# Performance work log

Hardware: AMD Instinct MI355X
Metric: run time of the kernel (lower is better)

Reference implementation:

```python
import jax, jax.numpy as jnp
import numpy as np

H, HD, RD = 16, 128, 64          # n_heads, head_dim, rope_dim
CD = HD - RD                      # content_dim = 64
THETA = 10000.0


def apply_rope(x, cos, sin):
    # x: [B,H,T,RD]; cos/sin: [T,RD//2] broadcast over B,H
    d = x.shape[-1] // 2
    x1, x2 = x[..., :d], x[..., d:]
    return jnp.concatenate([x1 * cos - x2 * sin, x1 * sin + x2 * cos], axis=-1)


def setup_inputs() -> dict:
    key = jax.random.key(0)
    ks = jax.random.split(key, 9)
    d_model, q_rank, d_latent = 2048, 512, 512
    B, T = 2, 2048
    s = 0.02
    return {
        "x": jax.random.normal(ks[0], (B, T, d_model), dtype=jnp.float32),
        "Wq_down": jax.random.normal(ks[1], (d_model, q_rank), dtype=jnp.float32) * s,
        "Wq_up": jax.random.normal(ks[2], (q_rank, H * CD), dtype=jnp.float32) * s,
        "Wq_rope": jax.random.normal(ks[3], (d_model, H * RD), dtype=jnp.float32) * s,
        "Wkv_down": jax.random.normal(ks[4], (d_model, d_latent), dtype=jnp.float32) * s,
        "Wk_up": jax.random.normal(ks[5], (d_latent, H * CD), dtype=jnp.float32) * s,
        "Wv_up": jax.random.normal(ks[6], (d_latent, H * HD), dtype=jnp.float32) * s,
        "Wk_rope": jax.random.normal(ks[7], (d_model, H * RD), dtype=jnp.float32) * s,
        "Wo": jax.random.normal(ks[8], (H * HD, d_model), dtype=jnp.float32) * s,
    }


def reference(x, Wq_down, Wq_up, Wq_rope, Wkv_down, Wk_up, Wv_up, Wk_rope, Wo):
    B, T, _ = x.shape

    # low-rank projections
    q_content = (x @ Wq_down) @ Wq_up            # [B,T,H*CD]
    q_pos = x @ Wq_rope                          # [B,T,H*RD]
    kv_latent = x @ Wkv_down                     # [B,T,d_latent]
    k_content = kv_latent @ Wk_up                # [B,T,H*CD]
    k_pos = x @ Wk_rope                          # [B,T,H*RD]
    v = kv_latent @ Wv_up                        # [B,T,H*HD]

    def split_heads(t, d):
        return t.reshape(B, T, H, d).transpose(0, 2, 1, 3)  # [B,H,T,d]

    q_content = split_heads(q_content, CD)
    q_pos = split_heads(q_pos, RD)
    k_content = split_heads(k_content, CD)
    k_pos = split_heads(k_pos, RD)
    v = split_heads(v, HD)

    # rotary tables: [T, RD//2]
    inv_freq = 1.0 / (THETA ** (jnp.arange(0, RD, 2, dtype=jnp.float32) / RD))
    freqs = jnp.arange(T, dtype=jnp.float32)[:, None] * inv_freq[None, :]
    cos, sin = jnp.cos(freqs), jnp.sin(freqs)

    q_pos = apply_rope(q_pos, cos, sin)
    k_pos = apply_rope(k_pos, cos, sin)

    q = jnp.concatenate([q_content, q_pos], axis=-1)  # [B,H,T,HD]
    k = jnp.concatenate([k_content, k_pos], axis=-1)  # [B,H,T,HD]

    # causal SDPA, scale = 1/sqrt(head_dim)
    scale = 1.0 / jnp.sqrt(jnp.asarray(HD, dtype=q.dtype))
    scores = jnp.einsum("bhqd,bhkd->bhqk", q, k) * scale
    causal = jnp.tril(jnp.ones((T, T), dtype=bool))
    scores = jnp.where(causal, scores, jnp.finfo(scores.dtype).min)
    attn = jax.nn.softmax(scores, axis=-1)
    out = jnp.einsum("bhqk,bhkd->bhqd", attn, v)      # [B,H,T,HD]

    out = out.transpose(0, 2, 1, 3).reshape(B, T, H * HD)
    return out @ Wo
```

## Files before the change

kernel.cpp:

```cpp
#include <hip/hip_runtime.h>
#include <hip/hip_bf16.h>
#include <stdint.h>
#include <math.h>

#define H_ 16
#define HD_ 128
#define RD_ 64
#define CD_ 64
#define DM_ 2048
#define QR_ 512
#define DL_ 512
#define B_ 2
#define T_ 2048
#define M_TOT (B_*T_)

typedef __attribute__((ext_vector_type(8))) short short8;
typedef __attribute__((ext_vector_type(4))) float f32x4;
typedef __attribute__((ext_vector_type(16))) float f32x16;

__device__ __forceinline__ unsigned short f2b_hw(float f){
  __hip_bfloat16 h = __float2bfloat16(f);
  union { __hip_bfloat16 h; unsigned short u; } c; c.h = h; return c.u;
}
__device__ __forceinline__ float b2f(unsigned short b){
  union { unsigned u; float f; } a; a.u = ((unsigned)b) << 16;
  return a.f;
}

#define GLOAD16(g, l) __builtin_amdgcn_global_load_lds( \
    (__attribute__((address_space(1))) void*)(g), \
    (__attribute__((address_space(3))) void*)(l), 16, 0, 0)

__global__ void cast_f32_bf16(const float* __restrict__ src,
                              unsigned short* __restrict__ dst, int n){
  int i = (blockIdx.x * blockDim.x + threadIdx.x) * 4;
  if (i < n){
    float4 v = *(const float4*)(src + i);
    ushort4 o;
    o.x = f2b_hw(v.x); o.y = f2b_hw(v.y); o.z = f2b_hw(v.z); o.w = f2b_hw(v.w);
    *(ushort4*)(dst + i) = o;
  }
}

struct TTe { const float* src; unsigned short* dst; int K, N, blk0; };
struct TT8 { TTe e[8]; };

__global__ void transpose_cast8(TT8 tab){
  __shared__ float tile[32][33];
  int bid = blockIdx.x;
  const float* src = tab.e[0].src;
  unsigned short* dst = tab.e[0].dst;
  int K = tab.e[0].K, N = tab.e[0].N, loc = bid;
  #pragma unroll
  for (int j = 1; j < 8; j++){
    if (bid >= tab.e[j].blk0){
      src = tab.e[j].src; dst = tab.e[j].dst;
      K = tab.e[j].K; N = tab.e[j].N; loc = bid - tab.e[j].blk0;
    }
  }
  int cols = N / 32;
  int n0 = (loc % cols) * 32, k0 = (loc / cols) * 32;
  int tx = threadIdx.x, ty = threadIdx.y;
  #pragma unroll
  for (int r = ty; r < 32; r += 8)
    tile[r][tx] = src[(size_t)(k0 + r) * N + n0 + tx];
  __syncthreads();
  #pragma unroll
  for (int r = ty; r < 32; r += 8)
    dst[(size_t)(n0 + r) * K + k0 + tx] = f2b_hw(tile[tx][r]);
}

template<int OUTF32>
__global__ __launch_bounds__(256) void gemm_bt(
    const unsigned short* __restrict__ A, int lda,
    const unsigned short* __restrict__ Bt,
    void* __restrict__ Cv, int ldc, int N, int K)
{
  __shared__ unsigned short As[128 * 32];
  __shared__ unsigned short Bs[128 * 32];
  int tid = threadIdx.x;

  int gx = gridDim.x;
  int nwg = gx * gridDim.y;
  int lin = blockIdx.x + gx * blockIdx.y;
  int q8 = nwg >> 3;
  int nl = (lin & 7) * q8 + (lin >> 3);
  int m0 = (nl / gx) * 128, n0 = (nl % gx) * 128;

  int lane = tid & 63, w = tid >> 6;
  int wr = (w >> 1) * 64, wc = (w & 1) * 64;
  int mr = lane & 15, kg = lane >> 4;

  const unsigned short* Ag = A  + (size_t)(m0 + (tid >> 2)) * lda + ((tid & 3) << 3);
  const unsigned short* Bg = Bt + (size_t)(n0 + (tid >> 2)) * K + ((tid & 3) << 3);

  f32x4 acc[4][4];
  #pragma unroll
  for (int i = 0; i < 4; i++)
    #pragma unroll
    for (int j = 0; j < 4; j++)
      acc[i][j] = (f32x4){0.f, 0.f, 0.f, 0.f};

  for (int k0 = 0; k0 < K; k0 += 32) {
    #pragma unroll
    for (int j = 0; j < 2; j++) {
      GLOAD16(Ag + (size_t)j * 64 * lda, &As[j * 2048 + tid * 8]);
      GLOAD16(Bg + (size_t)j * 64 * K, &Bs[j * 2048 + tid * 8]);
    }
    Ag += 32; Bg += 32;
    __syncthreads();
    short8 af[4], bf[4];
    #pragma unroll
    for (int i = 0; i < 4; i++)
      af[i] = *(const short8*)&As[(wr + i * 16 + mr) * 32 + kg * 8];
    #pragma unroll
    for (int j = 0; j < 4; j++)
      bf[j] = *(const short8*)&Bs[(wc + j * 16 + mr) * 32 + kg * 8];
    __builtin_amdgcn_s_setprio(1);
    #pragma unroll
    for (int i = 0; i < 4; i++)
      #pragma unroll
      for (int j = 0; j < 4; j++)
        acc[i][j] = __builtin_amdgcn_mfma_f32_16x16x32_bf16(af[i], bf[j], acc[i][j], 0, 0, 0);
    __builtin_amdgcn_s_setprio(0);
    __syncthreads();
  }

  if (OUTF32) {
    float* C = (float*)Cv;
    #pragma unroll
    for (int i = 0; i < 4; i++)
      #pragma unroll
      for (int j = 0; j < 4; j++)
        #pragma unroll
        for (int r = 0; r < 4; r++) {
          int row = m0 + wr + i * 16 + kg * 4 + r;
          int col = n0 + wc + j * 16 + mr;
          C[(size_t)row * ldc + col] = acc[i][j][r];
        }
  } else {
    unsigned short* C = (unsigned short*)Cv;
    #pragma unroll
    for (int i = 0; i < 4; i++)
      #pragma unroll
      for (int j = 0; j < 4; j++)
        #pragma unroll
        for (int r = 0; r < 4; r++) {
          int row = m0 + wr + i * 16 + kg * 4 + r;
          int col = n0 + wc + j * 16 + mr;
          C[(size_t)row * ldc + col] = f2b_hw(acc[i][j][r]);
        }
  }
}

__global__ void assemble_qk(const unsigned short* __restrict__ qc,
                            const unsigned short* __restrict__ projall,
                            const unsigned short* __restrict__ kcv,
                            unsigned short* __restrict__ qh,
                            unsigned short* __restrict__ kh){
  int row = blockIdx.x * 2 + threadIdx.y;
  int d = threadIdx.x;
  int bh = row >> 11;
  int t  = row & (T_ - 1);
  int b = bh / H_, h = bh % H_;
  size_t srow = (size_t)b * T_ + t;
  size_t dst = ((size_t)bh * T_ + t) * 128 + d;
  if (d < 64) {
    qh[dst] = qc[srow * 1024 + h * 64 + d];
    kh[dst] = kcv[srow * 3072 + h * 64 + d];
  } else {
    int i = d - 64;
    int j = i & 31;
    float invf = exp2f(-(float)j * 0.4152410118750f);
    float f = (float)t * invf;
    float s, c;
    sincosf(f, &s, &c);
    float qx1 = b2f(projall[srow * 3072 + 1024 + h * 64 + j]);
    float qx2 = b2f(projall[srow * 3072 + 1024 + h * 64 + j + 32]);
    float kx1 = b2f(projall[srow * 3072 + 2048 + h * 64 + j]);
    float kx2 = b2f(projall[srow * 3072 + 2048 + h * 64 + j + 32]);
    float qv = (i < 32) ? (qx1 * c - qx2 * s) : (qx1 * s + qx2 * c);
    float kv = (i < 32) ? (kx1 * c - kx2 * s) : (kx1 * s + kx2 * c);
    qh[dst] = f2b_hw(qv);
    kh[dst] = f2b_hw(kv);
  }
}

__global__ void vtrans(const unsigned short* __restrict__ kcv,
                       unsigned short* __restrict__ vt){
  __shared__ unsigned short tile[32][33];
  int bh = blockIdx.z;
  int b = bh / H_, h = bh % H_;
  const unsigned short* src = kcv + (size_t)b * T_ * 3072 + 1024 + h * HD_;
  unsigned short* dst = vt + (size_t)bh * HD_ * T_;
  int t0 = blockIdx.x * 32, d0 = blockIdx.y * 32;
  int tx = threadIdx.x, ty = threadIdx.y;
  #pragma unroll
  for (int r = ty; r < 32; r += 8)
    tile[r][tx] = src[(size_t)(t0 + r) * 3072 + d0 + tx];
  __syncthreads();
  #pragma unroll
  for (int r = ty; r < 32; r += 8)
    dst[(size_t)(d0 + r) * T_ + t0 + tx] = tile[tx][r];
}

__global__ __launch_bounds__(256, 2) void attn_fwd3(
    const unsigned short* __restrict__ qh,
    const unsigned short* __restrict__ kh,
    const unsigned short* __restrict__ vt,
    unsigned short* __restrict__ ao)
{
  __shared__ __align__(16) unsigned short Ks[2][64 * 128];
  __shared__ __align__(16) unsigned short Vs[2][128 * 64];

  const int tid  = threadIdx.x;
  const int lane = tid & 63, w = tid >> 6;
  const int l31  = lane & 31, hi = lane >> 5;
  const int bh = blockIdx.y;
  const int b  = bh >> 4, hd = bh & 15;
  int qt = blockIdx.x;
  if (blockIdx.y >= 16) qt = 15 - qt;
  const int q0    = qt * 128;
  const int q0w   = q0 + w * 32;
  const int qg    = q0w + l31;
  const int qmaxw = q0w + 31;
  const int nt    = 2 * qt + 2;

  const unsigned short* Qg = qh + (size_t)bh * T_ * 128;
  const unsigned short* Kg = kh + (size_t)bh * T_ * 128;
  const unsigned short* Vg = vt + (size_t)bh * 128 * T_;

  short8 qf[8];
  #pragma unroll
  for (int kc = 0; kc < 8; kc++)
    qf[kc] = *(const short8*)&Qg[(size_t)qg * 128 + kc * 16 + hi * 8];

  f32x16 accO[4];
  #pragma unroll
  for (int sb = 0; sb < 4; sb++)
    #pragma unroll
    for (int r = 0; r < 16; r++) accO[sb][r] = 0.f;

  float m = -1e30f, lsum = 0.f;
  const float SC = 0.12751743f;

  int krow[4], kwof[4], vrow[4], vwof[4];
  #pragma unroll
  for (int j = 0; j < 4; j++){
    int r_ = (w * 4 + j) * 4 + (lane >> 4);
    krow[j] = r_;
    kwof[j] = r_ * 128 + ((((lane & 15) * 16) ^ ((r_ & 7) << 4)) >> 1);
    int d_ = (w * 4 + j) * 8 + (lane >> 3);
    vrow[j] = d_;
    vwof[j] = d_ * 64 + ((((lane & 7) * 16) ^ ((d_ & 7) << 4)) >> 1);
  }
  const int kcol = (lane & 15) * 8;
  const int vcol = (lane & 7) * 8;

  uint4 kst[4], vst[4];

#define REG_LOAD(kvt) do {                                                    \
    int kv0s = (kvt) * 64;                                                    \
    _Pragma("unroll")                                                         \
    for (int j_ = 0; j_ < 4; j_++) {                                          \
      kst[j_] = *(const uint4*)&Kg[(size_t)(kv0s + krow[j_]) * 128 + kcol];   \
      vst[j_] = *(const uint4*)&Vg[(size_t)vrow[j_] * T_ + kv0s + vcol];      \
    }                                                                         \
  } while (0)

#define DS_WRITE(bufi) do {                                                   \
    _Pragma("unroll")                                                         \
    for (int j_ = 0; j_ < 4; j_++) {                                          \
      *(uint4*)&Ks[bufi][kwof[j_]] = kst[j_];                                 \
      *(uint4*)&Vs[bufi][vwof[j_]] = vst[j_];                                 \
    }                                                                         \
  } while (0)

  REG_LOAD(0);
  DS_WRITE(0);
  if (nt > 1) REG_LOAD(1);
  asm volatile("s_waitcnt lgkmcnt(0)" ::: "memory");
  __builtin_amdgcn_s_barrier();
  __builtin_amdgcn_sched_barrier(0);

  for (int t = 0; t < nt; t++) {
    const int cur = t & 1;
    if (t + 1 < nt) DS_WRITE(cur ^ 1);
    if (t + 2 < nt) REG_LOAD(t + 2);
    const int kv0 = t * 64;
    if (kv0 <= qmaxw) {
      const unsigned short* Kb = &Ks[cur][0];
      const unsigned short* Vb = &Vs[cur][0];

      f32x16 sa0, sa1;
      #pragma unroll
      for (int r = 0; r < 16; r++) { sa0[r] = 0.f; sa1[r] = 0.f; }
      __builtin_amdgcn_s_setprio(1);
      #pragma unroll
      for (int kc = 0; kc < 8; kc++) {
        int co = (kc * 32 + hi * 16);
        int r0 = l31;
        short8 kf0 = *(const short8*)&Kb[r0 * 128 + ((co ^ ((r0 & 7) << 4)) >> 1)];
        sa0 = __builtin_amdgcn_mfma_f32_32x32x16_bf16(kf0, qf[kc], sa0, 0, 0, 0);
        int r1 = 32 + l31;
        short8 kf1 = *(const short8*)&Kb[r1 * 128 + ((co ^ ((r1 & 7) << 4)) >> 1)];
        sa1 = __builtin_amdgcn_mfma_f32_32x32x16_bf16(kf1, qf[kc], sa1, 0, 0, 0);
      }
      __builtin_amdgcn_s_setprio(0);

      float p0[16], p1[16];
      float pmax = -1e30f;
      bool needMask = (kv0 + 63 > q0w);
      if (needMask) {
        #pragma unroll
        for (int r = 0; r < 16; r++) {
          int crow = (r & 3) + 8 * (r >> 2) + 4 * hi;
          float v0 = sa0[r] * SC;
          float v1 = sa1[r] * SC;
          if (kv0 + crow > qg)      v0 = -1e30f;
          if (kv0 + 32 + crow > qg) v1 = -1e30f;
          p0[r] = v0; p1[r] = v1;
          pmax = fmaxf(pmax, fmaxf(v0, v1));
        }
      } else {
        #pragma unroll
        for (int r = 0; r < 16; r++) {
          float v0 = sa0[r] * SC;
          float v1 = sa1[r] * SC;
          p0[r] = v0; p1[r] = v1;
          pmax = fmaxf(pmax, fmaxf(v0, v1));
        }
      }
      pmax = fmaxf(pmax, __shfl_xor(pmax, 32, 64));
      if (!__all(pmax <= m + 8.f)) {
        float mn  = fmaxf(m, pmax);
        float fac = exp2f(m - mn);
        m = mn;
        lsum *= fac;
        #pragma unroll
        for (int sb = 0; sb < 4; sb++)
          #pragma unroll
          for (int r = 0; r < 16; r++) accO[sb][r] *= fac;
      }
      float ls = 0.f;
      #pragma unroll
      for (int r = 0; r < 16; r++) {
        p0[r] = exp2f(p0[r] - m);
        p1[r] = exp2f(p1[r] - m);
        ls += p0[r] + p1[r];
      }
      ls += __shfl_xor(ls, 32, 64);
      lsum += ls;

      #pragma unroll
      for (int kc2 = 0; kc2 < 4; kc2++) {
        const int c2 = kc2 & 1;
        short8 pa;
        #pragma unroll
        for (int j = 0; j < 4; j++) {
          float a  = (kc2 < 2) ? p0[8 * c2 + j]     : p1[8 * c2 + j];
          float bv = (kc2 < 2) ? p0[8 * c2 + 4 + j] : p1[8 * c2 + 4 + j];
          float snd = hi ? a : bv;
          float rcv = __shfl_xor(snd, 32, 64);
          float lo = hi ? rcv : a;
          float hh = hi ? bv : rcv;
          pa[j]     = (short)f2b_hw(lo);
          pa[4 + j] = (short)f2b_hw(hh);
        }
        __builtin_amdgcn_s_setprio(1);
        #pragma unroll
        for (int sb = 0; sb < 4; sb++) {
          int d = sb * 32 + l31;
          short8 vf = *(const short8*)&Vb[d * 64 + (((kc2 * 32 + hi * 16) ^ ((d & 7) << 4)) >> 1)];
          accO[sb] = __builtin_amdgcn_mfma_f32_32x32x16_bf16(vf, pa, accO[sb], 0, 0, 0);
        }
        __builtin_amdgcn_s_setprio(0);
      }
    }
    __builtin_amdgcn_sched_barrier(0);
    asm volatile("s_waitcnt lgkmcnt(0)" ::: "memory");
    __builtin_amdgcn_s_barrier();
    __builtin_amdgcn_sched_barrier(0);
  }

  float rl = 1.0f / lsum;
  size_t orow = ((size_t)b * T_ + qg) * (H_*HD_) + hd * 128;
  #pragma unroll
  for (int sb = 0; sb < 4; sb++)
    #pragma unroll
    for (int g = 0; g < 4; g++) {
      ushort4 o;
      o.x = f2b_hw(accO[sb][4 * g + 0] * rl);
      o.y = f2b_hw(accO[sb][4 * g + 1] * rl);
      o.z = f2b_hw(accO[sb][4 * g + 2] * rl);
      o.w = f2b_hw(accO[sb][4 * g + 3] * rl);
      *(ushort4*)&ao[orow + sb * 32 + 8 * g + 4 * hi] = o;
    }
#undef REG_LOAD
#undef DS_WRITE
}

extern "C" void kernel_launch(void* const* d_in, const int* in_sizes, int n_in,
                              void* d_out, int out_size, void* d_ws, size_t ws_size,
                              hipStream_t stream)
{
  (void)in_sizes; (void)n_in; (void)out_size; (void)ws_size;
  const float* x        = (const float*)d_in[0];
  const float* Wq_down  = (const float*)d_in[1];
  const float* Wq_up    = (const float*)d_in[2];
  const float* Wq_rope  = (const float*)d_in[3];
  const float* Wkv_down = (const float*)d_in[4];
  const float* Wk_up    = (const float*)d_in[5];
  const float* Wv_up    = (const float*)d_in[6];
  const float* Wk_rope  = (const float*)d_in[7];
  const float* Wo       = (const float*)d_in[8];

  char* ws = (char*)d_ws;
  unsigned short* xb      = (unsigned short*)(ws + 0);
  unsigned short* Wdall   = (unsigned short*)(ws + 16777216);
  unsigned short* WquT    = (unsigned short*)(ws + 29360128);
  unsigned short* WkcvT   = (unsigned short*)(ws + 30408704);
  unsigned short* WoT     = (unsigned short*)(ws + 33554432);
  unsigned short* projall = (unsigned short*)(ws + 41943040);
  unsigned short* qcbuf   = (unsigned short*)(ws + 67108864);
  unsigned short* kcvbuf  = (unsigned short*)(ws + 75497472);
  unsigned short* qh      = (unsigned short*)(ws + 100663296);
  unsigned short* kh      = (unsigned short*)(ws + 117440512);
  unsigned short* vt      = (unsigned short*)(ws + 134217728);
  unsigned short* ao      = projall;

  dim3 tb(32, 8);

  cast_f32_bf16<<<(M_TOT * DM_ / 4 + 255) / 256, 256, 0, stream>>>(x, xb, M_TOT * DM_);

  TT8 tab;
  int blk = 0;
  tab.e[0] = { Wq_down,  Wdall,               DM_, QR_,     blk }; blk += (QR_/32)*(DM_/32);
  tab.e[1] = { Wkv_down, Wdall + 512*2048,    DM_, DL_,     blk }; blk += (DL_/32)*(DM_/32);
  tab.e[2] = { Wq_rope,  Wdall + 1024*2048,   DM_, H_*RD_,  blk }; blk += (H_*RD_/32)*(DM_/32);
  tab.e[3] = { Wk_rope,  Wdall + 2048*2048,   DM_, H_*RD_,  blk }; blk += (H_*RD_/32)*(DM_/32);
  tab.e[4] = { Wq_up,    WquT,                QR_, H_*CD_,  blk }; blk += (H_*CD_/32)*(QR_/32);
  tab.e[5] = { Wk_up,    WkcvT,               DL_, H_*CD_,  blk }; blk += (H_*CD_/32)*(DL_/32);
  tab.e[6] = { Wv_up,    WkcvT + 1024*512,    DL_, H_*HD_,  blk }; blk += (H_*HD_/32)*(DL_/32);
  tab.e[7] = { Wo,       WoT,                 H_*HD_, DM_,  blk }; blk += (DM_/32)*(H_*HD_/32);
  transpose_cast8<<<blk, tb, 0, stream>>>(tab);

  gemm_bt<0><<<dim3(3072/128, M_TOT/128), 256, 0, stream>>>(xb, DM_, Wdall, projall, 3072, 3072, DM_);
  gemm_bt<0><<<dim3(1024/128, M_TOT/128), 256, 0, stream>>>(projall, 3072, WquT, qcbuf, 1024, 1024, QR_);
  gemm_bt<0><<<dim3(3072/128, M_TOT/128), 256, 0, stream>>>(projall + 512, 3072, WkcvT, kcvbuf, 3072, 3072, DL_);

  assemble_qk<<<dim3(B_*H_*T_/2), dim3(128, 2), 0, stream>>>(qcbuf, projall, kcvbuf, qh, kh);
  vtrans<<<dim3(T_/32, HD_/32, B_*H_), tb, 0, stream>>>(kcvbuf, vt);

  attn_fwd3<<<dim3(16, 32), 256, 0, stream>>>(qh, kh, vt, ao);

  gemm_bt<1><<<dim3(DM_/128, M_TOT/128), 256, 0, stream>>>(ao, 2048, WoT, d_out, DM_, DM_, H_*HD_);
}
```

Before: 350.6 us.

## Fuse head-split and V transpose into GEMM epilogues; single-buffer V in attention

```diff
diff --git a/kernel.cpp b/kernel.cpp
--- a/kernel.cpp
+++ b/kernel.cpp
@@ -26,6 +26,10 @@
   union { unsigned u; float f; } a; a.u = ((unsigned)b) << 16;
   return a.f;
 }
+__device__ __forceinline__ unsigned pack2(float lo, float hi){
+  __hip_bfloat162 h2 = __float22bfloat162_rn(make_float2(lo, hi));
+  union { __hip_bfloat162 h; unsigned u; } c; c.h = h2; return c.u;
+}
 
 #define GLOAD16(g, l) __builtin_amdgcn_global_load_lds( \
     (__attribute__((address_space(1))) void*)(g), \
@@ -70,11 +74,11 @@
     dst[(size_t)(n0 + r) * K + k0 + tx] = f2b_hw(tile[tx][r]);
 }
 
-template<int OUTF32>
+template<int MODE>
 __global__ __launch_bounds__(256) void gemm_bt(
     const unsigned short* __restrict__ A, int lda,
     const unsigned short* __restrict__ Bt,
-    void* __restrict__ Cv, int ldc, int N, int K)
+    void* __restrict__ Cv, void* __restrict__ Cv2, int ldc, int N, int K)
 {
   __shared__ unsigned short As[128 * 32];
   __shared__ unsigned short Bs[128 * 32];
@@ -126,7 +130,7 @@
     __syncthreads();
   }
 
-  if (OUTF32) {
+  if (MODE == 1) {
     float* C = (float*)Cv;
     #pragma unroll
     for (int i = 0; i < 4; i++)
@@ -138,7 +142,7 @@
           int col = n0 + wc + j * 16 + mr;
           C[(size_t)row * ldc + col] = acc[i][j][r];
         }
-  } else {
+  } else if (MODE == 0) {
     unsigned short* C = (unsigned short*)Cv;
     #pragma unroll
     for (int i = 0; i < 4; i++)
@@ -150,68 +154,89 @@
           int col = n0 + wc + j * 16 + mr;
           C[(size_t)row * ldc + col] = f2b_hw(acc[i][j][r]);
         }
-  }
-}
-
-__global__ void assemble_qk(const unsigned short* __restrict__ qc,
-                            const unsigned short* __restrict__ projall,
-                            const unsigned short* __restrict__ kcv,
-                            unsigned short* __restrict__ qh,
-                            unsigned short* __restrict__ kh){
-  int row = blockIdx.x * 2 + threadIdx.y;
-  int d = threadIdx.x;
+  } else if (MODE == 2) {
+    unsigned short* qhp = (unsigned short*)Cv;
+    #pragma unroll
+    for (int i = 0; i < 4; i++)
+      #pragma unroll
+      for (int j = 0; j < 4; j++) {
+        int colb = n0 + wc + j * 16 + mr;
+        int h = colb >> 6, d = colb & 63;
+        #pragma unroll
+        for (int r = 0; r < 4; r++) {
+          int gr = m0 + wr + i * 16 + kg * 4 + r;
+          size_t idx = ((size_t)((gr >> 11) * H_ + h) * T_ + (gr & (T_-1))) * 128 + d;
+          qhp[idx] = f2b_hw(acc[i][j][r]);
+        }
+      }
+  } else {
+    unsigned short* khp = (unsigned short*)Cv;
+    unsigned short* vtp = (unsigned short*)Cv2;
+    if (n0 < 1024) {
+      #pragma unroll
+      for (int i = 0; i < 4; i++)
+        #pragma unroll
+        for (int j = 0; j < 4; j++) {
+          int colb = n0 + wc + j * 16 + mr;
+          int h = colb >> 6, d = colb & 63;
+          #pragma unroll
+          for (int r = 0; r < 4; r++) {
+            int gr = m0 + wr + i * 16 + kg * 4 + r;
+            size_t idx = ((size_t)((gr >> 11) * H_ + h) * T_ + (gr & (T_-1))) * 128 + d;
+            khp[idx] = f2b_hw(acc[i][j][r]);
+          }
+        }
+    } else {
+      #pragma unroll
+      for (int i = 0; i < 4; i++)
+        #pragma unroll
+        for (int j = 0; j < 4; j++) {
+          int c2 = n0 + wc + j * 16 + mr - 1024;
+          int h = c2 >> 7, d = c2 & 127;
+          int gr0 = m0 + wr + i * 16 + kg * 4;
+          int b = gr0 >> 11, t0 = gr0 & (T_-1);
+          ushort4 o;
+          o.x = f2b_hw(acc[i][j][0]); o.y = f2b_hw(acc[i][j][1]);
+          o.z = f2b_hw(acc[i][j][2]); o.w = f2b_hw(acc[i][j][3]);
+          size_t idx = ((size_t)(b * H_ + h) * 128 + d) * T_ + t0;
+          *(ushort4*)&vtp[idx] = o;
+        }
+    }
+  }
+}
+
+__global__ void rope_fill(const unsigned short* __restrict__ projall,
+                          unsigned short* __restrict__ qh,
+                          unsigned short* __restrict__ kh){
+  int row = blockIdx.x * 8 + threadIdx.y;
+  int j = threadIdx.x;
   int bh = row >> 11;
   int t  = row & (T_ - 1);
-  int b = bh / H_, h = bh % H_;
+  int b = bh >> 4, h = bh & 15;
   size_t srow = (size_t)b * T_ + t;
-  size_t dst = ((size_t)bh * T_ + t) * 128 + d;
-  if (d < 64) {
-    qh[dst] = qc[srow * 1024 + h * 64 + d];
-    kh[dst] = kcv[srow * 3072 + h * 64 + d];
-  } else {
-    int i = d - 64;
-    int j = i & 31;
-    float invf = exp2f(-(float)j * 0.4152410118750f);
-    float f = (float)t * invf;
-    float s, c;
-    sincosf(f, &s, &c);
-    float qx1 = b2f(projall[srow * 3072 + 1024 + h * 64 + j]);
-    float qx2 = b2f(projall[srow * 3072 + 1024 + h * 64 + j + 32]);
-    float kx1 = b2f(projall[srow * 3072 + 2048 + h * 64 + j]);
-    float kx2 = b2f(projall[srow * 3072 + 2048 + h * 64 + j + 32]);
-    float qv = (i < 32) ? (qx1 * c - qx2 * s) : (qx1 * s + qx2 * c);
-    float kv = (i < 32) ? (kx1 * c - kx2 * s) : (kx1 * s + kx2 * c);
-    qh[dst] = f2b_hw(qv);
-    kh[dst] = f2b_hw(kv);
-  }
-}
-
-__global__ void vtrans(const unsigned short* __restrict__ kcv,
-                       unsigned short* __restrict__ vt){
-  __shared__ unsigned short tile[32][33];
-  int bh = blockIdx.z;
-  int b = bh / H_, h = bh % H_;
-  const unsigned short* src = kcv + (size_t)b * T_ * 3072 + 1024 + h * HD_;
-  unsigned short* dst = vt + (size_t)bh * HD_ * T_;
-  int t0 = blockIdx.x * 32, d0 = blockIdx.y * 32;
-  int tx = threadIdx.x, ty = threadIdx.y;
-  #pragma unroll
-  for (int r = ty; r < 32; r += 8)
-    tile[r][tx] = src[(size_t)(t0 + r) * 3072 + d0 + tx];
-  __syncthreads();
-  #pragma unroll
-  for (int r = ty; r < 32; r += 8)
-    dst[(size_t)(d0 + r) * T_ + t0 + tx] = tile[tx][r];
-}
-
-__global__ __launch_bounds__(256, 2) void attn_fwd3(
+  const unsigned short* qp = projall + srow * 3072 + 1024 + h * 64;
+  const unsigned short* kp = qp + 1024;
+  float invf = exp2f(-(float)j * 0.4152410118750f);
+  float f = (float)t * invf;
+  float s, c;
+  sincosf(f, &s, &c);
+  float qx1 = b2f(qp[j]), qx2 = b2f(qp[j + 32]);
+  float kx1 = b2f(kp[j]), kx2 = b2f(kp[j + 32]);
+  size_t dst = ((size_t)bh * T_ + t) * 128 + 64;
+  qh[dst + j]      = f2b_hw(qx1 * c - qx2 * s);
+  qh[dst + j + 32] = f2b_hw(qx1 * s + qx2 * c);
+  kh[dst + j]      = f2b_hw(kx1 * c - kx2 * s);
+  kh[dst + j + 32] = f2b_hw(kx1 * s + kx2 * c);
+}
+
+__global__ __launch_bounds__(256, 3) void attn_fwd4(
     const unsigned short* __restrict__ qh,
     const unsigned short* __restrict__ kh,
     const unsigned short* __restrict__ vt,
     unsigned short* __restrict__ ao)
 {
-  __shared__ __align__(16) unsigned short Ks[2][64 * 128];
-  __shared__ __align__(16) unsigned short Vs[2][128 * 64];
+  __shared__ __align__(16) unsigned short lds[3 * 8192];
+  unsigned short* const Vsp = lds + 16384;
 
   const int tid  = threadIdx.x;
   const int lane = tid & 63, w = tid >> 6;
@@ -259,38 +284,49 @@
 
   uint4 kst[4], vst[4];
 
-#define REG_LOAD(kvt) do {                                                    \
+#define REG_LOAD_K(kvt) do {                                                  \
     int kv0s = (kvt) * 64;                                                    \
     _Pragma("unroll")                                                         \
-    for (int j_ = 0; j_ < 4; j_++) {                                          \
+    for (int j_ = 0; j_ < 4; j_++)                                            \
       kst[j_] = *(const uint4*)&Kg[(size_t)(kv0s + krow[j_]) * 128 + kcol];   \
+  } while (0)
+#define REG_LOAD_V(kvt) do {                                                  \
+    int kv0s = (kvt) * 64;                                                    \
+    _Pragma("unroll")                                                         \
+    for (int j_ = 0; j_ < 4; j_++)                                            \
       vst[j_] = *(const uint4*)&Vg[(size_t)vrow[j_] * T_ + kv0s + vcol];      \
-    }                                                                         \
   } while (0)
-
-#define DS_WRITE(bufi) do {                                                   \
+#define DS_WRITE_K(bufi) do {                                                 \
+    unsigned short* ksb_ = lds + (bufi) * 8192;                               \
     _Pragma("unroll")                                                         \
-    for (int j_ = 0; j_ < 4; j_++) {                                          \
-      *(uint4*)&Ks[bufi][kwof[j_]] = kst[j_];                                 \
-      *(uint4*)&Vs[bufi][vwof[j_]] = vst[j_];                                 \
-    }                                                                         \
+    for (int j_ = 0; j_ < 4; j_++)                                            \
+      *(uint4*)&ksb_[kwof[j_]] = kst[j_];                                     \
   } while (0)
-
-  REG_LOAD(0);
-  DS_WRITE(0);
-  if (nt > 1) REG_LOAD(1);
-  asm volatile("s_waitcnt lgkmcnt(0)" ::: "memory");
-  __builtin_amdgcn_s_barrier();
-  __builtin_amdgcn_sched_barrier(0);
+#define DS_WRITE_V() do {                                                     \
+    _Pragma("unroll")                                                         \
+    for (int j_ = 0; j_ < 4; j_++)                                            \
+      *(uint4*)&Vsp[vwof[j_]] = vst[j_];                                      \
+  } while (0)
+
+  REG_LOAD_K(0);
+  REG_LOAD_V(0);
+  DS_WRITE_K(0);
+  if (nt > 1) REG_LOAD_K(1);
 
   for (int t = 0; t < nt; t++) {
     const int cur = t & 1;
-    if (t + 1 < nt) DS_WRITE(cur ^ 1);
-    if (t + 2 < nt) REG_LOAD(t + 2);
-    const int kv0 = t * 64;
-    if (kv0 <= qmaxw) {
-      const unsigned short* Kb = &Ks[cur][0];
-      const unsigned short* Vb = &Vs[cur][0];
+    DS_WRITE_V();
+    if (t + 1 < nt) DS_WRITE_K(cur ^ 1);
+    if (t + 1 < nt) REG_LOAD_V(t + 1);
+    if (t + 2 < nt) REG_LOAD_K(t + 2);
+    __builtin_amdgcn_sched_barrier(0);
+    asm volatile("s_waitcnt lgkmcnt(0)" ::: "memory");
+    __builtin_amdgcn_s_barrier();
+    __builtin_amdgcn_sched_barrier(0);
+
+    if (t * 64 <= qmaxw) {
+      const int kv0 = t * 64;
+      const unsigned short* Kb = lds + cur * 8192;
 
       f32x16 sa0, sa1;
       #pragma unroll
@@ -354,24 +390,25 @@
 
       #pragma unroll
       for (int kc2 = 0; kc2 < 4; kc2++) {
-        const int c2 = kc2 & 1;
-        short8 pa;
-        #pragma unroll
-        for (int j = 0; j < 4; j++) {
-          float a  = (kc2 < 2) ? p0[8 * c2 + j]     : p1[8 * c2 + j];
-          float bv = (kc2 < 2) ? p0[8 * c2 + 4 + j] : p1[8 * c2 + 4 + j];
-          float snd = hi ? a : bv;
-          float rcv = __shfl_xor(snd, 32, 64);
-          float lo = hi ? rcv : a;
-          float hh = hi ? bv : rcv;
-          pa[j]     = (short)f2b_hw(lo);
-          pa[4 + j] = (short)f2b_hw(hh);
-        }
+        unsigned A01, A23, B01, B23;
+        if (kc2 == 0) { A01 = pack2(p0[0], p0[1]);  A23 = pack2(p0[2], p0[3]);
+                        B01 = pack2(p0[4], p0[5]);  B23 = pack2(p0[6], p0[7]); }
+        else if (kc2 == 1) { A01 = pack2(p0[8], p0[9]);   A23 = pack2(p0[10], p0[11]);
+                             B01 = pack2(p0[12], p0[13]); B23 = pack2(p0[14], p0[15]); }
+        else if (kc2 == 2) { A01 = pack2(p1[0], p1[1]);  A23 = pack2(p1[2], p1[3]);
+                             B01 = pack2(p1[4], p1[5]);  B23 = pack2(p1[6], p1[7]); }
+        else { A01 = pack2(p1[8], p1[9]);   A23 = pack2(p1[10], p1[11]);
+               B01 = pack2(p1[12], p1[13]); B23 = pack2(p1[14], p1[15]); }
+        asm("v_permlane32_swap_b32 %0, %1" : "+v"(A01), "+v"(B01));
+        asm("v_permlane32_swap_b32 %0, %1" : "+v"(A23), "+v"(B23));
+        union { unsigned u[4]; short8 v; } pk;
+        pk.u[0] = A01; pk.u[1] = A23; pk.u[2] = B01; pk.u[3] = B23;
+        short8 pa = pk.v;
         __builtin_amdgcn_s_setprio(1);
         #pragma unroll
         for (int sb = 0; sb < 4; sb++) {
           int d = sb * 32 + l31;
-          short8 vf = *(const short8*)&Vb[d * 64 + (((kc2 * 32 + hi * 16) ^ ((d & 7) << 4)) >> 1)];
+          short8 vf = *(const short8*)&Vsp[d * 64 + (((kc2 * 32 + hi * 16) ^ ((d & 7) << 4)) >> 1)];
           accO[sb] = __builtin_amdgcn_mfma_f32_32x32x16_bf16(vf, pa, accO[sb], 0, 0, 0);
         }
         __builtin_amdgcn_s_setprio(0);
@@ -396,8 +433,10 @@
       o.w = f2b_hw(accO[sb][4 * g + 3] * rl);
       *(ushort4*)&ao[orow + sb * 32 + 8 * g + 4 * hi] = o;
     }
-#undef REG_LOAD
-#undef DS_WRITE
+#undef REG_LOAD_K
+#undef REG_LOAD_V
+#undef DS_WRITE_K
+#undef DS_WRITE_V
 }
 
 extern "C" void kernel_launch(void* const* d_in, const int* in_sizes, int n_in,
@@ -422,11 +461,9 @@
   unsigned short* WkcvT   = (unsigned short*)(ws + 30408704);
   unsigned short* WoT     = (unsigned short*)(ws + 33554432);
   unsigned short* projall = (unsigned short*)(ws + 41943040);
-  unsigned short* qcbuf   = (unsigned short*)(ws + 67108864);
-  unsigned short* kcvbuf  = (unsigned short*)(ws + 75497472);
-  unsigned short* qh      = (unsigned short*)(ws + 100663296);
-  unsigned short* kh      = (unsigned short*)(ws + 117440512);
-  unsigned short* vt      = (unsigned short*)(ws + 134217728);
+  unsigned short* qh      = (unsigned short*)(ws + 67108864);
+  unsigned short* kh      = (unsigned short*)(ws + 83886080);
+  unsigned short* vt      = (unsigned short*)(ws + 100663296);
   unsigned short* ao      = projall;
 
   dim3 tb(32, 8);
@@ -445,14 +482,12 @@
   tab.e[7] = { Wo,       WoT,                 H_*HD_, DM_,  blk }; blk += (DM_/32)*(H_*HD_/32);
   transpose_cast8<<<blk, tb, 0, stream>>>(tab);
 
-  gemm_bt<0><<<dim3(3072/128, M_TOT/128), 256, 0, stream>>>(xb, DM_, Wdall, projall, 3072, 3072, DM_);
-  gemm_bt<0><<<dim3(1024/128, M_TOT/128), 256, 0, stream>>>(projall, 3072, WquT, qcbuf, 1024, 1024, QR_);
-  gemm_bt<0><<<dim3(3072/128, M_TOT/128), 256, 0, stream>>>(projall + 512, 3072, WkcvT, kcvbuf, 3072, 3072, DL_);
-
-  assemble_qk<<<dim3(B_*H_*T_/2), dim3(128, 2), 0, stream>>>(qcbuf, projall, kcvbuf, qh, kh);
-  vtrans<<<dim3(T_/32, HD_/32, B_*H_), tb, 0, stream>>>(kcvbuf, vt);
-
-  attn_fwd3<<<dim3(16, 32), 256, 0, stream>>>(qh, kh, vt, ao);
-
-  gemm_bt<1><<<dim3(DM_/128, M_TOT/128), 256, 0, stream>>>(ao, 2048, WoT, d_out, DM_, DM_, H_*HD_);
-}
+  gemm_bt<0><<<dim3(3072/128, M_TOT/128), 256, 0, stream>>>(xb, DM_, Wdall, projall, nullptr, 3072, 3072, DM_);
+  gemm_bt<2><<<dim3(1024/128, M_TOT/128), 256, 0, stream>>>(projall, 3072, WquT, qh, nullptr, 0, 1024, QR_);
+  gemm_bt<3><<<dim3(3072/128, M_TOT/128), 256, 0, stream>>>(projall + 512, 3072, WkcvT, kh, vt, 0, 3072, DL_);
+  rope_fill<<<dim3(B_*H_*T_/8), dim3(32, 8), 0, stream>>>(projall, qh, kh);
+
+  attn_fwd4<<<dim3(16, 32), 256, 0, stream>>>(qh, kh, vt, ao);
+
+  gemm_bt<1><<<dim3(DM_/128, M_TOT/128), 256, 0, stream>>>(ao, 2048, WoT, d_out, nullptr, DM_, DM_, H_*HD_);
+}
```

After: 488.1 us. 1.39x slower.
